# Optimization experiments

Measured on AMD Instinct MI355X. Metric: run time of the kernel, lower is better.

The kernel has to match this reference:

```python
import jax, jax.numpy as jnp
import numpy as np
from jax import lax

WINDOW = 11
SIGMA = 1.5
CHANNELS = 3
DATA_RANGE = 1.0
WEIGHTS = (0.0448, 0.2856, 0.3001, 0.2363, 0.1333)


def _gaussian_kernel_2d(size, sigma, channels):
    x = np.arange(size, dtype=np.float32) - size // 2
    k1 = np.exp(-x ** 2 / (2 * sigma ** 2))
    k1 = k1 / k1.sum()
    k2 = np.outer(k1, k1)
    k2 = k2 / k2.sum()
    return jnp.asarray(np.tile(k2[None, None], (channels, 1, 1, 1)), dtype=jnp.float32)


def _depthwise_blur(x, kernel):
    # x: [B, G, H, W], kernel: [C, 1, kh, kw] tiled to G groups
    groups = x.shape[1]
    reps = groups // kernel.shape[0]
    k = jnp.tile(kernel, (reps, 1, 1, 1))
    return lax.conv_general_dilated(
        x, k, window_strides=(1, 1), padding='SAME',
        feature_group_count=groups,
        dimension_numbers=('NCHW', 'OIHW', 'NCHW'))


def _avg_pool2(x):
    b, c, h, w = x.shape
    return x.reshape(b, c, h // 2, 2, w // 2, 2).mean(axis=(3, 5))


def _ssim_components(pred, target, kernel):
    C1 = (0.01 * DATA_RANGE) ** 2
    C2 = (0.03 * DATA_RANGE) ** 2
    # Fuse the 5 depthwise blurs into a single grouped conv over stacked channels
    stacked = jnp.concatenate(
        [pred, target, pred * pred, target * target, pred * target], axis=1)
    blurred = _depthwise_blur(stacked, kernel)
    mu1, mu2, e_pp, e_tt, e_pt = jnp.split(blurred, 5, axis=1)
    mu1_sq = mu1 * mu1
    mu2_sq = mu2 * mu2
    mu1_mu2 = mu1 * mu2
    sigma1_sq = jnp.maximum(e_pp - mu1_sq, 0.0)
    sigma2_sq = jnp.maximum(e_tt - mu2_sq, 0.0)
    sigma12 = e_pt - mu1_mu2
    l = (2 * mu1_mu2 + C1) / (mu1_sq + mu2_sq + C1)
    cs = (2 * sigma12 + C2) / (sigma1_sq + sigma2_sq + C2)
    return l.mean(), cs.mean()


def setup_inputs() -> dict:
    key = jax.random.key(0)
    k1, k2 = jax.random.split(key)
    pred = jax.random.uniform(k1, (16, 3, 512, 512), dtype=jnp.float32)
    target = jax.random.uniform(k2, (16, 3, 512, 512), dtype=jnp.float32)
    kernel = _gaussian_kernel_2d(WINDOW, SIGMA, CHANNELS)
    return {'pred': pred, 'target': target, 'kernel': kernel}


def reference(pred, target, kernel):
    weights = jnp.asarray(WEIGHTS, dtype=pred.dtype)
    msssim = jnp.ones((1,), dtype=pred.dtype)
    n_scales = len(WEIGHTS)
    for i in range(n_scales):
        if i > 0:
            pred = _avg_pool2(pred)
            target = _avg_pool2(target)
        if pred.shape[2] < WINDOW or pred.shape[3] < WINDOW:
            break
        l, cs = _ssim_components(pred, target, kernel)
        if i == n_scales - 1:
            msssim = msssim * jnp.maximum(l, 1e-8) ** weights[i] \
                            * jnp.maximum(cs, 1e-8) ** weights[i]
        else:
            msssim = msssim * jnp.maximum(cs, 1e-8) ** weights[i]
    return msssim
```

## Files before the change

kernel.cpp:

```cpp
#include <hip/hip_runtime.h>
#include <math.h>

#define NP 48

typedef float v2f __attribute__((ext_vector_type(2)));

__device__ __forceinline__ float uniform_f(float v) {
    int i = __builtin_amdgcn_readfirstlane(__builtin_bit_cast(int, v));
    return __builtin_bit_cast(float, i);
}

__device__ __forceinline__ void ssim_scale(
        const float* __restrict__ P, const float* __restrict__ T,
        int H, int sh, int lb, int scale, int slotsel, int tid,
        const float* __restrict__ k2d, double* __restrict__ accum)
{
    float w[11];
    {
        float s = 0.f;
#pragma unroll
        for (int i = 0; i < 11; ++i) s += k2d[55 + i];
        float inv = 1.0f / s;
#pragma unroll
        for (int i = 0; i < 11; ++i) w[i] = uniform_f(k2d[55 + i] * inv);
    }

    int blocksX = (NP << sh) >> 8;
    int bxi = lb % blocksX;
    int by  = lb / blocksX;
    int g   = (bxi << 8) + tid;
    int pl  = g >> sh;
    int x   = g & (H - 1);
    int yb  = by * 32;

    int bcl = x - 5;
    bcl = bcl < 0 ? 0 : bcl;
    bcl = bcl > H - 11 ? H - 11 : bcl;
    int d = bcl - (x - 5);
    float wc[11];
#pragma unroll
    for (int j = 0; j < 11; ++j) {
        int idx = j + d;
        float val = 0.f;
#pragma unroll
        for (int i = 0; i < 11; ++i) val = (idx == i) ? w[i] : val;
        wc[j] = val;
    }

    const float* Pb = P + (size_t)pl * H * H + bcl;
    const float* Tb = T + (size_t)pl * H * H + bcl;

    v2f tap[2][11];
    v2f wmu[11], we[11];
    float wpt[11];
    const float C1 = 1e-4f, C2 = 9e-4f;
    float lsum = 0.f, csum = 0.f;
    int rr = yb - 5;

    {
        int cr = rr < 0 ? 0 : rr;
        const float* rp = Pb + (size_t)cr * H;
        const float* rt = Tb + (size_t)cr * H;
#pragma unroll
        for (int j = 0; j < 11; ++j) tap[0][j] = (v2f){rp[j], rt[j]};
    }

    for (int ch = 0; ch < 2; ++ch) {
#pragma unroll
        for (int ph = 0; ph < 22; ++ph) {
            const int cb = ph & 1;
            const int sl = ph % 11;

            {
                int nr = rr + 1;
                nr = nr < 0 ? 0 : nr;
                nr = nr > H - 1 ? H - 1 : nr;
                const float* rp = Pb + (size_t)nr * H;
                const float* rt = Tb + (size_t)nr * H;
#pragma unroll
                for (int j = 0; j < 11; ++j) tap[cb ^ 1][j] = (v2f){rp[j], rt[j]};
            }

            bool live = rr < yb + 37;
            v2f a_mu = (v2f){0.f, 0.f};
            v2f a_e  = (v2f){0.f, 0.f};
            v2f a_pt = (v2f){0.f, 0.f};
            if (live && rr >= 0 && rr < H) {
#pragma unroll
                for (int j = 0; j < 11; ++j) {
                    v2f pt2 = tap[cb][j];
                    v2f wv  = (v2f){wc[j], wc[j]};
                    v2f wp2 = wv * pt2;
                    v2f ptr2 = (v2f){pt2.y, pt2.x};
                    a_mu += wp2;
                    a_e  += wp2 * pt2;
                    a_pt += wp2 * ptr2;
                }
            }
            wmu[sl] = a_mu; we[sl] = a_e;
            wpt[sl] = a_pt.x + a_pt.y;

            if (live && rr >= yb + 5) {
                v2f mu2 = (v2f){0.f, 0.f};
                v2f e2  = (v2f){0.f, 0.f};
                float ept = 0.f;
#pragma unroll
                for (int i = 0; i < 11; ++i) {
                    const int ss = (sl + 1 + i) % 11;
                    v2f wi = (v2f){w[i], w[i]};
                    mu2 += wi * wmu[ss];
                    e2  += wi * we[ss];
                    ept += w[i] * wpt[ss];
                }
                float m11 = mu2.x * mu2.x, m22 = mu2.y * mu2.y, m12 = mu2.x * mu2.y;
                float s1  = fmaxf(e2.x - m11, 0.f);
                float s2  = fmaxf(e2.y - m22, 0.f);
                float s12 = 0.5f * ept - m12;
                lsum += (2.f * m12 + C1) * __builtin_amdgcn_rcpf(m11 + m22 + C1);
                csum += (2.f * s12 + C2) * __builtin_amdgcn_rcpf(s1 + s2 + C2);
            }
            rr++;
        }
    }

#pragma unroll
    for (int o = 32; o > 0; o >>= 1) {
        lsum += __shfl_down(lsum, o, 64);
        csum += __shfl_down(csum, o, 64);
    }
    __shared__ float red[8];
    int wv = tid >> 6;
    if ((tid & 63) == 0) { red[2 * wv] = lsum; red[2 * wv + 1] = csum; }
    __syncthreads();
    if (tid == 0) {
        int slot = (scale * 8 + slotsel) * 2;
        atomicAdd(&accum[slot],     (double)(red[0] + red[2] + red[4] + red[6]));
        atomicAdd(&accum[slot + 1], (double)(red[1] + red[3] + red[5] + red[7]));
    }
}

__global__ __launch_bounds__(256) void k_main(
        const float* __restrict__ pred, const float* __restrict__ targ,
        float* __restrict__ p1, float* __restrict__ t1,
        float* __restrict__ p2, float* __restrict__ t2,
        float* __restrict__ p3, float* __restrict__ t3,
        float* __restrict__ p4, float* __restrict__ t4,
        const float* __restrict__ k2d, double* __restrict__ accum) {
    int b   = blockIdx.x;
    int tid = threadIdx.x;
    if (b >= 1536) {
        ssim_scale(pred, targ, 512, 9, b - 1536, 0, b & 7, tid, k2d, accum);
        return;
    }
    int pi   = b >> 4;
    int tile = b & 15;
    int pls  = pi < 48 ? pi : pi - 48;
    const float* src = (pi < 48 ? pred : targ) + (size_t)pls * 512 * 512;
    float* d1 = (pi < 48 ? p1 : t1) + (size_t)pls * 256 * 256;
    float* d2 = (pi < 48 ? p2 : t2) + (size_t)pls * 128 * 128;
    float* d3 = (pi < 48 ? p3 : t3) + (size_t)pls * 64 * 64;
    float* d4 = (pi < 48 ? p4 : t4) + (size_t)pls * 32 * 32;
    int tY = tile >> 2, tX = tile & 3;
    int ty = tid >> 4, tx = tid & 15;
    int gy0 = tY * 128 + ty * 8, gx0 = tX * 128 + tx * 8;

    float s1v[4][4];
#pragma unroll
    for (int i = 0; i < 4; ++i) {
        const float* r0 = src + (size_t)(gy0 + 2 * i) * 512 + gx0;
        const float* r1 = r0 + 512;
        float4 a0 = *(const float4*)r0, a1 = *(const float4*)(r0 + 4);
        float4 b0 = *(const float4*)r1, b1 = *(const float4*)(r1 + 4);
        s1v[i][0] = 0.25f * ((a0.x + a0.y) + (b0.x + b0.y));
        s1v[i][1] = 0.25f * ((a0.z + a0.w) + (b0.z + b0.w));
        s1v[i][2] = 0.25f * ((a1.x + a1.y) + (b1.x + b1.y));
        s1v[i][3] = 0.25f * ((a1.z + a1.w) + (b1.z + b1.w));
        *(float4*)(d1 + (size_t)(tY * 64 + ty * 4 + i) * 256 + tX * 64 + tx * 4) =
            *(float4*)s1v[i];
    }
    float s2v[2][2];
#pragma unroll
    for (int i = 0; i < 2; ++i) {
#pragma unroll
        for (int j = 0; j < 2; ++j)
            s2v[i][j] = 0.25f * ((s1v[2*i][2*j] + s1v[2*i][2*j+1]) +
                                 (s1v[2*i+1][2*j] + s1v[2*i+1][2*j+1]));
        *(float2*)(d2 + (size_t)(tY * 32 + ty * 2 + i) * 128 + tX * 32 + tx * 2) =
            *(float2*)s2v[i];
    }
    float s3 = 0.25f * ((s2v[0][0] + s2v[0][1]) + (s2v[1][0] + s2v[1][1]));
    d3[(size_t)(tY * 16 + ty) * 64 + tX * 16 + tx] = s3;
    float v1 = s3 + __shfl_xor(s3, 1, 64);
    float v2 = v1 + __shfl_xor(v1, 16, 64);
    if ((ty & 1) == 0 && (tx & 1) == 0)
        d4[(size_t)(tY * 8 + (ty >> 1)) * 32 + tX * 8 + (tx >> 1)] = 0.25f * v2;
}

__global__ __launch_bounds__(256) void k_ssim_rest(
        const float* __restrict__ p1, const float* __restrict__ t1,
        const float* __restrict__ p2, const float* __restrict__ t2,
        const float* __restrict__ p3, const float* __restrict__ t3,
        const float* __restrict__ p4, const float* __restrict__ t4,
        const float* __restrict__ k2d, double* __restrict__ accum) {
    int b   = blockIdx.x;
    int tid = threadIdx.x;
    if (b < 384)      ssim_scale(p1, t1, 256, 8, b,       1, b & 7, tid, k2d, accum);
    else if (b < 480) ssim_scale(p2, t2, 128, 7, b - 384, 2, b & 7, tid, k2d, accum);
    else if (b < 504) ssim_scale(p3, t3, 64,  6, b - 480, 3, b & 7, tid, k2d, accum);
    else              ssim_scale(p4, t4, 32,  5, b - 504, 4, b & 7, tid, k2d, accum);
}

__global__ void k_final(const double* __restrict__ accum, float* __restrict__ out) {
    if (threadIdx.x != 0 || blockIdx.x != 0) return;
    const float wts[5] = {0.0448f, 0.2856f, 0.3001f, 0.2363f, 0.1333f};
    float ms = 1.0f;
    int Hs = 512;
    for (int s = 0; s < 5; ++s) {
        double lt = 0.0, ct = 0.0;
        for (int k = 0; k < 8; ++k) {
            lt += accum[(s * 8 + k) * 2];
            ct += accum[(s * 8 + k) * 2 + 1];
        }
        float N  = 48.0f * (float)Hs * (float)Hs;
        float l  = (float)lt / N;
        float cs = fmaxf((float)ct / N, 1e-8f);
        if (s == 4) {
            l = fmaxf(l, 1e-8f);
            ms *= powf(l, wts[s]) * powf(cs, wts[s]);
        } else {
            ms *= powf(cs, wts[s]);
        }
        Hs >>= 1;
    }
    out[0] = ms;
}

extern "C" void kernel_launch(void* const* d_in, const int* in_sizes, int n_in,
                              void* d_out, int out_size, void* d_ws, size_t ws_size,
                              hipStream_t stream) {
    const float* pred = (const float*)d_in[0];
    const float* targ = (const float*)d_in[1];
    const float* kern = (const float*)d_in[2];
    float* out = (float*)d_out;

    char* ws = (char*)d_ws;
    double* accum = (double*)ws;
    size_t off = 1024;
    float* p1 = (float*)(ws + off); off += (size_t)NP * 256 * 256 * 4;
    float* t1 = (float*)(ws + off); off += (size_t)NP * 256 * 256 * 4;
    float* p2 = (float*)(ws + off); off += (size_t)NP * 128 * 128 * 4;
    float* t2 = (float*)(ws + off); off += (size_t)NP * 128 * 128 * 4;
    float* p3 = (float*)(ws + off); off += (size_t)NP * 64 * 64 * 4;
    float* t3 = (float*)(ws + off); off += (size_t)NP * 64 * 64 * 4;
    float* p4 = (float*)(ws + off); off += (size_t)NP * 32 * 32 * 4;
    float* t4 = (float*)(ws + off); off += (size_t)NP * 32 * 32 * 4;

    hipMemsetAsync(accum, 0, 640, stream);
    k_main<<<3072, 256, 0, stream>>>(pred, targ, p1, t1, p2, t2, p3, t3, p4, t4, kern, accum);
    k_ssim_rest<<<510, 256, 0, stream>>>(p1, t1, p2, t2, p3, t3, p4, t4, kern, accum);
    k_final<<<1, 1, 0, stream>>>(accum, out);
}
```

Baseline: 219.1 us.

## Fuse pooling, SSIM and finalize into one cooperative persistent kernel

Replaces the memset plus three launches with a single cooperative kernel. It runs the pyramid pooling jobs, synchronizes the whole grid, then runs the SSIM jobs for all scales, and finishes with a finalize step after a second grid sync. SSIM row tiles grow from 32 to 64 rows, which cuts the duplicated 10-row halo work. Scale 0 SSIM no longer overlaps the pooling phase, and the 1026 SSIM jobs spread unevenly over the 1024-block grid. If the cooperative launch fails, the code falls back to three separate launches.

```diff
diff --git a/kernel.cpp b/kernel.cpp
--- a/kernel.cpp
+++ b/kernel.cpp
@@ -1,5 +1,8 @@
 #include <hip/hip_runtime.h>
+#include <hip/hip_cooperative_groups.h>
 #include <math.h>
+
+namespace cg = cooperative_groups;
 
 #define NP 48
 
@@ -10,6 +13,7 @@
     return __builtin_bit_cast(float, i);
 }
 
+template<int CHF, int TAIL, int R>
 __device__ __forceinline__ void ssim_scale(
         const float* __restrict__ P, const float* __restrict__ T,
         int H, int sh, int lb, int scale, int slotsel, int tid,
@@ -31,7 +35,7 @@
     int g   = (bxi << 8) + tid;
     int pl  = g >> sh;
     int x   = g & (H - 1);
-    int yb  = by * 32;
+    int yb  = by * R;
 
     int bcl = x - 5;
     bcl = bcl < 0 ? 0 : bcl;
@@ -65,63 +69,66 @@
         for (int j = 0; j < 11; ++j) tap[0][j] = (v2f){rp[j], rt[j]};
     }
 
-    for (int ch = 0; ch < 2; ++ch) {
-#pragma unroll
-        for (int ph = 0; ph < 22; ++ph) {
-            const int cb = ph & 1;
-            const int sl = ph % 11;
-
-            {
-                int nr = rr + 1;
-                nr = nr < 0 ? 0 : nr;
-                nr = nr > H - 1 ? H - 1 : nr;
-                const float* rp = Pb + (size_t)nr * H;
-                const float* rt = Tb + (size_t)nr * H;
-#pragma unroll
-                for (int j = 0; j < 11; ++j) tap[cb ^ 1][j] = (v2f){rp[j], rt[j]};
-            }
-
-            bool live = rr < yb + 37;
-            v2f a_mu = (v2f){0.f, 0.f};
-            v2f a_e  = (v2f){0.f, 0.f};
-            v2f a_pt = (v2f){0.f, 0.f};
-            if (live && rr >= 0 && rr < H) {
-#pragma unroll
-                for (int j = 0; j < 11; ++j) {
-                    v2f pt2 = tap[cb][j];
-                    v2f wv  = (v2f){wc[j], wc[j]};
-                    v2f wp2 = wv * pt2;
-                    v2f ptr2 = (v2f){pt2.y, pt2.x};
-                    a_mu += wp2;
-                    a_e  += wp2 * pt2;
-                    a_pt += wp2 * ptr2;
-                }
-            }
-            wmu[sl] = a_mu; we[sl] = a_e;
-            wpt[sl] = a_pt.x + a_pt.y;
-
-            if (live && rr >= yb + 5) {
-                v2f mu2 = (v2f){0.f, 0.f};
-                v2f e2  = (v2f){0.f, 0.f};
-                float ept = 0.f;
-#pragma unroll
-                for (int i = 0; i < 11; ++i) {
-                    const int ss = (sl + 1 + i) % 11;
-                    v2f wi = (v2f){w[i], w[i]};
-                    mu2 += wi * wmu[ss];
-                    e2  += wi * we[ss];
-                    ept += w[i] * wpt[ss];
-                }
-                float m11 = mu2.x * mu2.x, m22 = mu2.y * mu2.y, m12 = mu2.x * mu2.y;
-                float s1  = fmaxf(e2.x - m11, 0.f);
-                float s2  = fmaxf(e2.y - m22, 0.f);
-                float s12 = 0.5f * ept - m12;
-                lsum += (2.f * m12 + C1) * __builtin_amdgcn_rcpf(m11 + m22 + C1);
-                csum += (2.f * s12 + C2) * __builtin_amdgcn_rcpf(s1 + s2 + C2);
-            }
-            rr++;
-        }
-    }
+#define SSIM_STEP(PH)                                                          \
+    {                                                                          \
+        const int cb = (PH) & 1;               \
+        const int sl = (PH) % 11;              \
+        {                  \
+            int nr = rr + 1;                                                   \
+            nr = nr < 0 ? 0 : nr;                                              \
+            nr = nr > H - 1 ? H - 1 : nr;                                      \
+            const float* rp = Pb + (size_t)nr * H;                             \
+            const float* rt = Tb + (size_t)nr * H;                             \
+            _Pragma("unroll")                                                  \
+            for (int j = 0; j < 11; ++j) tap[cb ^ 1][j] = (v2f){rp[j], rt[j]}; \
+        }                                                                      \
+        v2f a_mu = (v2f){0.f, 0.f};                                            \
+        v2f a_e  = (v2f){0.f, 0.f};                                            \
+        v2f a_pt = (v2f){0.f, 0.f};                                            \
+        if (rr >= 0 && rr < H) {               \
+            _Pragma("unroll")                                                  \
+            for (int j = 0; j < 11; ++j) {                                     \
+                v2f pt2 = tap[cb][j];                                          \
+                v2f wv  = (v2f){wc[j], wc[j]};                                 \
+                v2f wp2 = wv * pt2;                                            \
+                v2f ptr2 = (v2f){pt2.y, pt2.x};                                \
+                a_mu += wp2;                                                   \
+                a_e  += wp2 * pt2;                                             \
+                a_pt += wp2 * ptr2;                   \
+            }                                                                  \
+        }                                                                      \
+        wmu[sl] = a_mu; we[sl] = a_e;                                          \
+        wpt[sl] = a_pt.x + a_pt.y;                         \
+        if (rr >= yb + 5) {                          \
+            v2f mu2 = (v2f){0.f, 0.f};                                         \
+            v2f e2  = (v2f){0.f, 0.f};                                         \
+            float ept = 0.f;                                                   \
+            _Pragma("unroll")                                                  \
+            for (int i = 0; i < 11; ++i) {                                     \
+                const int ss = (sl + 1 + i) % 11;            \
+                v2f wi = (v2f){w[i], w[i]};                \
+                mu2 += wi * wmu[ss];                                           \
+                e2  += wi * we[ss];                                            \
+                ept += w[i] * wpt[ss];                                         \
+            }                                                                  \
+            float m11 = mu2.x * mu2.x, m22 = mu2.y * mu2.y, m12 = mu2.x * mu2.y; \
+            float s1  = fmaxf(e2.x - m11, 0.f);                                \
+            float s2  = fmaxf(e2.y - m22, 0.f);                                \
+            float s12 = 0.5f * ept - m12;                                      \
+            lsum += (2.f * m12 + C1) * __builtin_amdgcn_rcpf(m11 + m22 + C1);  \
+            csum += (2.f * s12 + C2) * __builtin_amdgcn_rcpf(s1 + s2 + C2);    \
+        }                                                                      \
+        rr++;                                                                  \
+    }
+
+#pragma unroll 1
+    for (int ch = 0; ch < CHF; ++ch) {
+#pragma unroll
+        for (int ph = 0; ph < 22; ++ph) SSIM_STEP(ph)
+    }
+#pragma unroll
+    for (int ph = 0; ph < TAIL; ++ph) SSIM_STEP(ph)
+#undef SSIM_STEP
 
 #pragma unroll
     for (int o = 32; o > 0; o >>= 1) {
@@ -137,21 +144,16 @@
         atomicAdd(&accum[slot],     (double)(red[0] + red[2] + red[4] + red[6]));
         atomicAdd(&accum[slot + 1], (double)(red[1] + red[3] + red[5] + red[7]));
     }
-}
-
-__global__ __launch_bounds__(256) void k_main(
+    __syncthreads();
+}
+
+__device__ __forceinline__ void pool_job(int b, int tid,
         const float* __restrict__ pred, const float* __restrict__ targ,
         float* __restrict__ p1, float* __restrict__ t1,
         float* __restrict__ p2, float* __restrict__ t2,
         float* __restrict__ p3, float* __restrict__ t3,
-        float* __restrict__ p4, float* __restrict__ t4,
-        const float* __restrict__ k2d, double* __restrict__ accum) {
-    int b   = blockIdx.x;
-    int tid = threadIdx.x;
-    if (b >= 1536) {
-        ssim_scale(pred, targ, 512, 9, b - 1536, 0, b & 7, tid, k2d, accum);
-        return;
-    }
+        float* __restrict__ p4, float* __restrict__ t4)
+{
     int pi   = b >> 4;
     int tile = b & 15;
     int pls  = pi < 48 ? pi : pi - 48;
@@ -196,22 +198,27 @@
         d4[(size_t)(tY * 8 + (ty >> 1)) * 32 + tX * 8 + (tx >> 1)] = 0.25f * v2;
 }
 
-__global__ __launch_bounds__(256) void k_ssim_rest(
+__device__ __forceinline__ void ssim_dispatch(int j, int tid,
+        const float* __restrict__ pred, const float* __restrict__ targ,
         const float* __restrict__ p1, const float* __restrict__ t1,
         const float* __restrict__ p2, const float* __restrict__ t2,
         const float* __restrict__ p3, const float* __restrict__ t3,
         const float* __restrict__ p4, const float* __restrict__ t4,
-        const float* __restrict__ k2d, double* __restrict__ accum) {
-    int b   = blockIdx.x;
-    int tid = threadIdx.x;
-    if (b < 384)      ssim_scale(p1, t1, 256, 8, b,       1, b & 7, tid, k2d, accum);
-    else if (b < 480) ssim_scale(p2, t2, 128, 7, b - 384, 2, b & 7, tid, k2d, accum);
-    else if (b < 504) ssim_scale(p3, t3, 64,  6, b - 480, 3, b & 7, tid, k2d, accum);
-    else              ssim_scale(p4, t4, 32,  5, b - 504, 4, b & 7, tid, k2d, accum);
-}
-
-__global__ void k_final(const double* __restrict__ accum, float* __restrict__ out) {
-    if (threadIdx.x != 0 || blockIdx.x != 0) return;
+        const float* __restrict__ k2d, double* __restrict__ accum)
+{
+    if (j < 1020) {
+        const float *P, *T; int H, sh, lb, scale;
+        if (j < 768)       { P = pred; T = targ; H = 512; sh = 9; lb = j;        scale = 0; }
+        else if (j < 960)  { P = p1;   T = t1;   H = 256; sh = 8; lb = j - 768;  scale = 1; }
+        else if (j < 1008) { P = p2;   T = t2;   H = 128; sh = 7; lb = j - 960;  scale = 2; }
+        else               { P = p3;   T = t3;   H = 64;  sh = 6; lb = j - 1008; scale = 3; }
+        ssim_scale<3, 8, 64>(P, T, H, sh, lb, scale, j & 7, tid, k2d, accum);
+    } else {
+        ssim_scale<1, 20, 32>(p4, t4, 32, 5, j - 1020, 4, j & 7, tid, k2d, accum);
+    }
+}
+
+__device__ void finalize(const double* __restrict__ accum, float* __restrict__ out) {
     const float wts[5] = {0.0448f, 0.2856f, 0.3001f, 0.2363f, 0.1333f};
     float ms = 1.0f;
     int Hs = 512;
@@ -235,6 +242,56 @@
     out[0] = ms;
 }
 
+__global__ __launch_bounds__(256, 4) void k_fused(
+        const float* __restrict__ pred, const float* __restrict__ targ,
+        float* __restrict__ p1, float* __restrict__ t1,
+        float* __restrict__ p2, float* __restrict__ t2,
+        float* __restrict__ p3, float* __restrict__ t3,
+        float* __restrict__ p4, float* __restrict__ t4,
+        const float* __restrict__ k2d, double* __restrict__ accum,
+        float* __restrict__ out)
+{
+    int tid = threadIdx.x;
+    if (blockIdx.x == 0 && tid < 80) accum[tid] = 0.0;
+    for (int j = blockIdx.x; j < 1536; j += gridDim.x)
+        pool_job(j, tid, pred, targ, p1, t1, p2, t2, p3, t3, p4, t4);
+    cg::this_grid().sync();
+    for (int j = blockIdx.x; j < 1026; j += gridDim.x)
+        ssim_dispatch(j, tid, pred, targ, p1, t1, p2, t2, p3, t3, p4, t4, k2d, accum);
+    cg::this_grid().sync();
+    if (blockIdx.x == 0 && tid == 0) finalize(accum, out);
+}
+
+__global__ __launch_bounds__(256) void k_pool(
+        const float* __restrict__ pred, const float* __restrict__ targ,
+        float* __restrict__ p1, float* __restrict__ t1,
+        float* __restrict__ p2, float* __restrict__ t2,
+        float* __restrict__ p3, float* __restrict__ t3,
+        float* __restrict__ p4, float* __restrict__ t4,
+        double* __restrict__ accum)
+{
+    int tid = threadIdx.x;
+    if (blockIdx.x == 0 && tid < 80) accum[tid] = 0.0;
+    pool_job(blockIdx.x, tid, pred, targ, p1, t1, p2, t2, p3, t3, p4, t4);
+}
+
+__global__ __launch_bounds__(256) void k_ssim_all(
+        const float* __restrict__ pred, const float* __restrict__ targ,
+        const float* __restrict__ p1, const float* __restrict__ t1,
+        const float* __restrict__ p2, const float* __restrict__ t2,
+        const float* __restrict__ p3, const float* __restrict__ t3,
+        const float* __restrict__ p4, const float* __restrict__ t4,
+        const float* __restrict__ k2d, double* __restrict__ accum)
+{
+    ssim_dispatch(blockIdx.x, threadIdx.x, pred, targ, p1, t1, p2, t2, p3, t3,
+                  p4, t4, k2d, accum);
+}
+
+__global__ void k_final(const double* __restrict__ accum, float* __restrict__ out) {
+    if (threadIdx.x != 0 || blockIdx.x != 0) return;
+    finalize(accum, out);
+}
+
 extern "C" void kernel_launch(void* const* d_in, const int* in_sizes, int n_in,
                               void* d_out, int out_size, void* d_ws, size_t ws_size,
                               hipStream_t stream) {
@@ -255,8 +312,18 @@
     float* p4 = (float*)(ws + off); off += (size_t)NP * 32 * 32 * 4;
     float* t4 = (float*)(ws + off); off += (size_t)NP * 32 * 32 * 4;
 
-    hipMemsetAsync(accum, 0, 640, stream);
-    k_main<<<3072, 256, 0, stream>>>(pred, targ, p1, t1, p2, t2, p3, t3, p4, t4, kern, accum);
-    k_ssim_rest<<<510, 256, 0, stream>>>(p1, t1, p2, t2, p3, t3, p4, t4, kern, accum);
-    k_final<<<1, 1, 0, stream>>>(accum, out);
-}
+    void* params[13] = {
+        (void*)&pred, (void*)&targ,
+        (void*)&p1, (void*)&t1, (void*)&p2, (void*)&t2,
+        (void*)&p3, (void*)&t3, (void*)&p4, (void*)&t4,
+        (void*)&kern, (void*)&accum, (void*)&out
+    };
+    hipError_t err = hipLaunchCooperativeKernel(
+        reinterpret_cast<void*>(k_fused), dim3(1024), dim3(256), params, 0, stream);
+    if (err != hipSuccess) {
+        k_pool<<<1536, 256, 0, stream>>>(pred, targ, p1, t1, p2, t2, p3, t3, p4, t4, accum);
+        k_ssim_all<<<1026, 256, 0, stream>>>(pred, targ, p1, t1, p2, t2, p3, t3,
+                                             p4, t4, kern, accum);
+        k_final<<<1, 1, 0, stream>>>(accum, out);
+    }
+}
```

After: 749.6 us. 3.42x slower.
